# Performance work log

Hardware: AMD Instinct MI355X
Metric: run time of the kernel (lower is better)

## Reference

```python
import jax, jax.numpy as jnp
import numpy as np

B, N_TOK, N_ATOM = 1, 1024, 4096
C_S, C_Z, C_ATOM, C_PAIR = 384, 128, 128, 16
N_QUERY, N_KEY = 32, 128
N_BLOCKS = N_ATOM // N_QUERY
EPS = 1e-5


def layer_norm_scale(x, w):
    # LayerNorm with create_offset=False (scale only)
    mu = jnp.mean(x, axis=-1, keepdims=True)
    var = jnp.mean(jnp.square(x - mu), axis=-1, keepdims=True)
    return (x - mu) * jax.lax.rsqrt(var + EPS) * w


def atom_to_token_idx(num_atoms):
    # num_atoms: [N_tok] int -> token index for each atom [N_ATOM]
    ends = jnp.cumsum(num_atoms)
    return jnp.searchsorted(ends, jnp.arange(N_ATOM), side='right')


def setup_inputs() -> dict:
    key = jax.random.key(0)
    ks = jax.random.split(key, 10)
    return {
        'token_mask': jnp.ones((B, N_TOK), jnp.float32),
        'num_atoms_per_token': jnp.full((B, N_TOK), N_ATOM // N_TOK, jnp.int32),
        'cl': jax.random.normal(ks[0], (B, N_ATOM, C_ATOM), jnp.float32),
        'plm': jax.random.normal(ks[1], (B, N_BLOCKS, N_QUERY, N_KEY, C_PAIR), jnp.float32),
        'si_trunk': jax.random.normal(ks[2], (B, N_TOK, C_S), jnp.float32),
        'zij_trunk': jax.random.normal(ks[3], (B, N_TOK, N_TOK, C_Z), jnp.float32),
        'rl': jax.random.normal(ks[4], (B, N_ATOM, 3), jnp.float32),
        'ln_s_w': jnp.ones((C_S,), jnp.float32),
        'W_s': jax.random.normal(ks[5], (C_S, C_ATOM), jnp.float32) * 0.02,
        'b_s': jnp.zeros((C_ATOM,), jnp.float32),
        'ln_z_w': jnp.ones((C_Z,), jnp.float32),
        'W_z': jax.random.normal(ks[6], (C_Z, C_PAIR), jnp.float32) * 0.02,
        'b_z': jnp.zeros((C_PAIR,), jnp.float32),
        'W_r': jax.random.normal(ks[7], (3, C_ATOM), jnp.float32) * 0.02,
        'b_r': jnp.zeros((C_ATOM,), jnp.float32),
        'n_query': N_QUERY,
        'n_key': N_KEY,
    }


def reference(token_mask, num_atoms_per_token, cl, plm, si_trunk, zij_trunk, rl,
              ln_s_w, W_s, b_s, ln_z_w, W_z, b_z, W_r, b_r, n_query, n_key):
    # --- single rep: LayerNorm + Linear, then token -> atom broadcast ---
    s = jnp.einsum('btc,cd->btd', layer_norm_scale(si_trunk, ln_s_w), W_s) + b_s
    s = s * token_mask[..., None]  # zero padded tokens
    tok = jax.vmap(atom_to_token_idx)(num_atoms_per_token)  # [B, N_ATOM]
    s_atoms = jnp.take_along_axis(s, tok[..., None], axis=1)  # [B, N_ATOM, c_atom]
    cl_out = cl + s_atoms

    # --- pair rep: LayerNorm + Linear, then pair -> local block gather ---
    z = jnp.einsum('bijc,cd->bijd', layer_norm_scale(zij_trunk, ln_z_w), W_z) + b_z
    n_blocks = N_ATOM // n_query
    q_idx = jnp.arange(n_blocks)[:, None] * n_query + jnp.arange(n_query)[None, :]
    k_off = n_query // 2 - n_key // 2  # key window centered on query block
    k_idx = jnp.arange(n_blocks)[:, None] * n_query + k_off + jnp.arange(n_key)[None, :]
    valid = ((k_idx >= 0) & (k_idx < N_ATOM)).astype(z.dtype)  # [L, n_key]
    k_idx_c = jnp.clip(k_idx, 0, N_ATOM - 1)
    tok_q = tok[:, q_idx]    # [B, L, n_query]
    tok_k = tok[:, k_idx_c]  # [B, L, n_key]

    def gather_blocks(zb, tq, tk):
        return zb[tq[:, :, None], tk[:, None, :]]  # [L, nq, nk, C_PAIR]

    z_blk = jax.vmap(gather_blocks)(z, tok_q, tok_k)
    z_blk = z_blk * valid[None, :, None, :, None]
    plm_out = plm + z_blk

    # --- noisy position projection ---
    ql = cl_out + jnp.einsum('bac,cd->bad', rl, W_r) + b_r
    return cl_out, plm_out, ql
```

## Files before the change

kernel.cpp:

```cpp
#include <hip/hip_runtime.h>

#define N_TOKS 1024
#define N_ATOMS 4096
#define CS 384
#define CZ 128
#define CATOM 128
#define CPAIR 16
#define NQ 32
#define NK 128
#define NBLK 128
#define KOFF (-48)
#define KSEG 32
#define NSEG (NK / KSEG)
#define NB_B (NBLK * NSEG)
#define NB_A 256
#define LN_EPS 1e-5f

union alignas(16) SMem {
    struct {
        float ztile[NQ * KSEG * CPAIR];
        int ends[N_TOKS];
        int tokq[NQ]; int tokk[KSEG];
        int qmap[NQ]; int kmap[KSEG];
        int uqtok[NQ]; int uktok[KSEG];
        float kvalid[KSEG];
        int uqk[2];
        int wsum[4];
    } b;
    struct {
        float xh[CS][4];
        float sacc[8][4][CATOM];
        float s_l[4][CATOM];
        int ends[N_TOKS];
        int wsum[4];
    } a;
};

__device__ __forceinline__ void scan_ends(const int* __restrict__ na, int* ends, int* wsum, int t) {
    int4 v = ((const int4*)na)[t];
    int e0 = v.x, e1 = e0 + v.y, e2 = e1 + v.z, e3 = e2 + v.w;
    int s = e3;
    int lane = t & 63, w = t >> 6;
    #pragma unroll
    for (int off = 1; off < 64; off <<= 1) {
        int u = __shfl_up(s, off);
        if (lane >= off) s += u;
    }
    if (lane == 63) wsum[w] = s;
    __syncthreads();
    int wbase = 0;
    #pragma unroll
    for (int i = 0; i < 4; i++) wbase += (i < w) ? wsum[i] : 0;
    int base = wbase + s - e3;
    ends[4 * t + 0] = base + e0;
    ends[4 * t + 1] = base + e1;
    ends[4 * t + 2] = base + e2;
    ends[4 * t + 3] = base + e3;
    __syncthreads();
}

__device__ __forceinline__ int bsearch_tok(const int* ends, int a) {
    int lo = 0, hi = N_TOKS - 1;
    while (lo < hi) { int mid = (lo + hi) >> 1; if (ends[mid] > a) hi = mid; else lo = mid + 1; }
    return lo;
}

__global__ __launch_bounds__(256) void k_all(
        const int* __restrict__ na, const float* __restrict__ si,
        const float* __restrict__ lnw, const float* __restrict__ Ws,
        const float* __restrict__ bs, const float* __restrict__ mask,
        const float* __restrict__ cl, const float* __restrict__ rl,
        const float* __restrict__ Wr, const float* __restrict__ br,
        const float* __restrict__ zij, const float* __restrict__ lnzw,
        const float* __restrict__ Wz, const float* __restrict__ bz,
        const float* __restrict__ plm,
        float* __restrict__ cl_out, float* __restrict__ ql, float* __restrict__ plm_out) {
    __shared__ SMem sm;
    int t = threadIdx.x;
    int x = blockIdx.x;

    if (x >= NB_B) {
        int b = x - NB_B, Tlo = b * 4;
        scan_ends(na, sm.a.ends, sm.a.wsum, t);
        {
            int tl = t >> 6, l = t & 63;
            const float4* row4 = (const float4*)(si + (size_t)(Tlo + tl) * CS);
            float4 v0 = row4[l];
            float4 v1 = make_float4(0.f, 0.f, 0.f, 0.f);
            if (l < 32) v1 = row4[64 + l];
            float sum = v0.x + v0.y + v0.z + v0.w + v1.x + v1.y + v1.z + v1.w;
            float sq = v0.x*v0.x + v0.y*v0.y + v0.z*v0.z + v0.w*v0.w
                     + v1.x*v1.x + v1.y*v1.y + v1.z*v1.z + v1.w*v1.w;
            #pragma unroll
            for (int m = 32; m >= 1; m >>= 1) { sum += __shfl_xor(sum, m); sq += __shfl_xor(sq, m); }
            float mu = sum * (1.f / CS);
            float rstd = rsqrtf(sq * (1.f / CS) - mu * mu + LN_EPS);
            float4 g0 = ((const float4*)lnw)[l];
            sm.a.xh[4*l+0][tl] = (v0.x - mu) * rstd * g0.x;
            sm.a.xh[4*l+1][tl] = (v0.y - mu) * rstd * g0.y;
            sm.a.xh[4*l+2][tl] = (v0.z - mu) * rstd * g0.z;
            sm.a.xh[4*l+3][tl] = (v0.w - mu) * rstd * g0.w;
            if (l < 32) {
                float4 g1 = ((const float4*)lnw)[64 + l];
                sm.a.xh[256+4*l+0][tl] = (v1.x - mu) * rstd * g1.x;
                sm.a.xh[256+4*l+1][tl] = (v1.y - mu) * rstd * g1.y;
                sm.a.xh[256+4*l+2][tl] = (v1.z - mu) * rstd * g1.z;
                sm.a.xh[256+4*l+3][tl] = (v1.w - mu) * rstd * g1.w;
            }
        }
        __syncthreads();
        {
            int d4 = t & 31, cc = t >> 5;
            float4 a0 = make_float4(0,0,0,0), a1 = a0, a2 = a0, a3 = a0;
            const float4* Ws4 = (const float4*)Ws;
            int c0 = 48 * cc;
            #pragma unroll 4
            for (int c = c0; c < c0 + 48; c++) {
                float4 w = Ws4[(size_t)c * 32 + d4];
                float4 xv = *(const float4*)&sm.a.xh[c][0];
                a0.x += xv.x * w.x; a0.y += xv.x * w.y; a0.z += xv.x * w.z; a0.w += xv.x * w.w;
                a1.x += xv.y * w.x; a1.y += xv.y * w.y; a1.z += xv.y * w.z; a1.w += xv.y * w.w;
                a2.x += xv.z * w.x; a2.y += xv.z * w.y; a2.z += xv.z * w.z; a2.w += xv.z * w.w;
                a3.x += xv.w * w.x; a3.y += xv.w * w.y; a3.z += xv.w * w.z; a3.w += xv.w * w.w;
            }
            *(float4*)&sm.a.sacc[cc][0][d4 * 4] = a0;
            *(float4*)&sm.a.sacc[cc][1][d4 * 4] = a1;
            *(float4*)&sm.a.sacc[cc][2][d4 * 4] = a2;
            *(float4*)&sm.a.sacc[cc][3][d4 * 4] = a3;
        }
        __syncthreads();
        if (t < 128) {
            int tk = t >> 5, d = t & 31;
            float4 a = make_float4(0,0,0,0);
            #pragma unroll
            for (int cc = 0; cc < 8; cc++) {
                float4 p = *(const float4*)&sm.a.sacc[cc][tk][d * 4];
                a.x += p.x; a.y += p.y; a.z += p.z; a.w += p.w;
            }
            float4 bb = ((const float4*)bs)[d];
            float m = mask[Tlo + tk];
            a.x = (a.x + bb.x) * m; a.y = (a.y + bb.y) * m;
            a.z = (a.z + bb.z) * m; a.w = (a.w + bb.w) * m;
            *(float4*)&sm.a.s_l[tk][d * 4] = a;
        }
        __syncthreads();
        int elo = (Tlo == 0) ? 0 : sm.a.ends[Tlo - 1];
        int e_0 = sm.a.ends[Tlo], e_1 = sm.a.ends[Tlo + 1], e_2 = sm.a.ends[Tlo + 2];
        int ehi = (b == NB_A - 1) ? N_ATOMS : sm.a.ends[Tlo + 3];
        elo = min(max(elo, 0), N_ATOMS);
        ehi = min(max(ehi, 0), N_ATOMS);
        if (ehi < elo) ehi = elo;
        int items = (ehi - elo) * 32;
        for (int i = t; i < items; i += 256) {
            int a = elo + (i >> 5), d = i & 31;
            int tk = (a >= e_0) + (a >= e_1) + (a >= e_2);
            float4 c4 = ((const float4*)cl)[(size_t)a * 32 + d];
            float4 sv = *(const float4*)&sm.a.s_l[tk][d * 4];
            float4 co;
            co.x = c4.x + sv.x; co.y = c4.y + sv.y; co.z = c4.z + sv.z; co.w = c4.w + sv.w;
            float px = rl[a * 3 + 0], py = rl[a * 3 + 1], pz = rl[a * 3 + 2];
            float4 w0 = ((const float4*)Wr)[d];
            float4 w1 = ((const float4*)Wr)[32 + d];
            float4 w2 = ((const float4*)Wr)[64 + d];
            float4 bb = ((const float4*)br)[d];
            float4 q;
            q.x = co.x + px * w0.x + py * w1.x + pz * w2.x + bb.x;
            q.y = co.y + px * w0.y + py * w1.y + pz * w2.y + bb.y;
            q.z = co.z + px * w0.z + py * w1.z + pz * w2.z + bb.z;
            q.w = co.w + px * w0.w + py * w1.w + pz * w2.w + bb.w;
            ((float4*)cl_out)[(size_t)a * 32 + d] = co;
            ((float4*)ql)[(size_t)a * 32 + d] = q;
        }
        return;
    }

    int blk = x >> 2, kseg = x & 3;
    scan_ends(na, sm.b.ends, sm.b.wsum, t);

    if (t < NQ) {
        sm.b.tokq[t] = bsearch_tok(sm.b.ends, blk * NQ + t);
    } else if (t >= 64 && t < 64 + KSEG) {
        int kk = t - 64;
        int kg = blk * NQ + KOFF + kseg * KSEG + kk;
        sm.b.kvalid[kk] = (kg >= 0 && kg < N_ATOMS) ? 1.0f : 0.0f;
        sm.b.tokk[kk] = bsearch_tok(sm.b.ends, min(max(kg, 0), N_ATOMS - 1));
    }
    __syncthreads();

    if (t < NQ) {
        int tq = sm.b.tokq[t];
        bool head = (t == 0) || (tq != sm.b.tokq[t - 1]);
        unsigned long long m = __ballot(head);
        int rank = (int)__popcll(m & ((2ull << t) - 1)) - 1;
        sm.b.qmap[t] = rank;
        if (head) sm.b.uqtok[rank] = tq;
        if (t == 0) sm.b.uqk[0] = (int)__popcll(m);
    } else if (t >= 64 && t < 64 + KSEG) {
        int lane = t - 64;
        int tk = sm.b.tokk[lane];
        bool head = (lane == 0) || (tk != sm.b.tokk[lane - 1]);
        unsigned long long m = __ballot(head);
        int rank = (int)__popcll(m & ((2ull << lane) - 1)) - 1;
        sm.b.kmap[lane] = rank;
        if (head) sm.b.uktok[rank] = tk;
        if (lane == 0) sm.b.uqk[1] = (int)__popcll(m);
    }
    __syncthreads();
    int uq = sm.b.uqk[0], uk = sm.b.uqk[1];
    int npairs = uq * uk;

    const float4* plm4 = (const float4*)plm;
    float4 pv[16];
    #pragma unroll
    for (int i = 0; i < 16; i++) {
        int f = t + i * 256;
        int d4 = f & 3;
        int kk = (f >> 2) & 31;
        int q  = f >> 7;
        size_t g = ((size_t)(blk * NQ + q) * NK + (size_t)kseg * KSEG + kk) * (CPAIR / 4) + d4;
        pv[i] = plm4[g];
    }

    for (int p = t; p < npairs; p += 256) {
        int qi = p / uk, ki = p - qi * uk;
        int tq = sm.b.uqtok[qi], tk = sm.b.uktok[ki];
        const float* row = zij + ((size_t)tq * N_TOKS + tk) * CZ;
        float sum = 0.f, sq = 0.f;
        for (int c4 = 0; c4 < CZ / 4; c4++) {
            float4 v = *(const float4*)(row + c4 * 4);
            sum += v.x + v.y + v.z + v.w;
            sq  += v.x * v.x + v.y * v.y + v.z * v.z + v.w * v.w;
        }
        float mu = sum * (1.f / CZ);
        float rstd = rsqrtf(sq * (1.f / CZ) - mu * mu + LN_EPS);
        float acc[CPAIR];
        #pragma unroll
        for (int d = 0; d < CPAIR; d++) acc[d] = bz[d];
        for (int c4 = 0; c4 < CZ / 4; c4++) {
            float4 v = *(const float4*)(row + c4 * 4);
            float xs4[4] = {v.x, v.y, v.z, v.w};
            #pragma unroll
            for (int j = 0; j < 4; j++) {
                int c = c4 * 4 + j;
                float xv = (xs4[j] - mu) * rstd * lnzw[c];
                const float* wrow = Wz + c * CPAIR;
                #pragma unroll
                for (int d = 0; d < CPAIR; d++) acc[d] += xv * wrow[d];
            }
        }
        float* zt = &sm.b.ztile[(qi * KSEG + ki) * CPAIR];
        #pragma unroll
        for (int d = 0; d < CPAIR; d++) zt[d] = acc[d];
    }
    __syncthreads();

    float4* out4 = (float4*)plm_out;
    #pragma unroll
    for (int i = 0; i < 16; i++) {
        int f = t + i * 256;
        int d4 = f & 3;
        int kk = (f >> 2) & 31;
        int q  = f >> 7;
        size_t g = ((size_t)(blk * NQ + q) * NK + (size_t)kseg * KSEG + kk) * (CPAIR / 4) + d4;
        float vd = sm.b.kvalid[kk];
        const float4 z = *(const float4*)&sm.b.ztile[(sm.b.qmap[q] * KSEG + sm.b.kmap[kk]) * CPAIR + d4 * 4];
        float4 v = pv[i];
        v.x += vd * z.x; v.y += vd * z.y; v.z += vd * z.z; v.w += vd * z.w;
        out4[g] = v;
    }
}

extern "C" void kernel_launch(void* const* d_in, const int* in_sizes, int n_in,
                              void* d_out, int out_size, void* d_ws, size_t ws_size,
                              hipStream_t stream) {
    (void)in_sizes; (void)n_in; (void)out_size; (void)d_ws; (void)ws_size;
    const float* token_mask = (const float*)d_in[0];
    const int*   num_atoms  = (const int*)d_in[1];
    const float* cl   = (const float*)d_in[2];
    const float* plm  = (const float*)d_in[3];
    const float* si   = (const float*)d_in[4];
    const float* zij  = (const float*)d_in[5];
    const float* rl   = (const float*)d_in[6];
    const float* ln_s_w = (const float*)d_in[7];
    const float* W_s  = (const float*)d_in[8];
    const float* b_s  = (const float*)d_in[9];
    const float* ln_z_w = (const float*)d_in[10];
    const float* W_z  = (const float*)d_in[11];
    const float* b_z  = (const float*)d_in[12];
    const float* W_r  = (const float*)d_in[13];
    const float* b_r  = (const float*)d_in[14];

    float* out_cl  = (float*)d_out;
    float* out_plm = out_cl + (size_t)N_ATOMS * CATOM;
    float* out_ql  = out_plm + (size_t)NBLK * NQ * NK * CPAIR;

    k_all<<<NB_B + NB_A, 256, 0, stream>>>(num_atoms, si, ln_s_w, W_s, b_s, token_mask,
                                           cl, rl, W_r, b_r,
                                           zij, ln_z_w, W_z, b_z, plm,
                                           out_cl, out_ql, out_plm);
}
```

Measured before the change: 40.00 us.

## Split pair LayerNorm-projection across 8 lanes per pair and halve key segments

Each unique token pair's 128-channel LayerNorm and 128x16 projection is now computed by 8 cooperating lanes, each handling 16 channels, with reductions done by cross-lane shuffles. Previously a single thread handled a whole pair. The key segment shrinks from 32 to 16, doubling the number of pair-path blocks, and the plm prefetch is moved ahead of the token scan so it overlaps with it. Pairs are processed in chunks of up to 256 through shared memory, with an extra sync per chunk. This adds shuffle overhead and recomputes some pairs across the finer segments.

```diff
diff --git a/kernel.cpp b/kernel.cpp
--- a/kernel.cpp
+++ b/kernel.cpp
@@ -10,15 +10,16 @@
 #define NK 128
 #define NBLK 128
 #define KOFF (-48)
-#define KSEG 32
+#define KSEG 16
 #define NSEG (NK / KSEG)
 #define NB_B (NBLK * NSEG)
 #define NB_A 256
+#define MAXP 256
 #define LN_EPS 1e-5f
 
 union alignas(16) SMem {
     struct {
-        float ztile[NQ * KSEG * CPAIR];
+        float ztile[MAXP * CPAIR];
         int ends[N_TOKS];
         int tokq[NQ]; int tokk[KSEG];
         int qmap[NQ]; int kmap[KSEG];
@@ -174,7 +175,20 @@
         return;
     }
 
-    int blk = x >> 2, kseg = x & 3;
+    int blk = x >> 3, kseg = x & 7;
+
+    const float4* plm4 = (const float4*)plm;
+    float4 pv[8];
+    #pragma unroll
+    for (int i = 0; i < 8; i++) {
+        int f = t + i * 256;
+        int d4 = f & 3;
+        int kk = (f >> 2) & 15;
+        int q  = f >> 6;
+        size_t g = ((size_t)(blk * NQ + q) * NK + (size_t)kseg * KSEG + kk) * (CPAIR / 4) + d4;
+        pv[i] = plm4[g];
+    }
+
     scan_ends(na, sm.b.ends, sm.b.wsum, t);
 
     if (t < NQ) {
@@ -209,64 +223,89 @@
     int uq = sm.b.uqk[0], uk = sm.b.uqk[1];
     int npairs = uq * uk;
 
-    const float4* plm4 = (const float4*)plm;
-    float4 pv[16];
+    int sl = t & 7;
+    const float4* bz4 = (const float4*)bz;
+    float4 bz0 = bz4[0], bz1 = bz4[1], bz2 = bz4[2], bz3 = bz4[3];
+
+    for (int c0 = 0; c0 < npairs; c0 += MAXP) {
+        int cend = min(npairs, c0 + MAXP);
+        for (int p = c0 + (t >> 3); p < cend; p += 32) {
+            int qi = p / uk, ki = p - qi * uk;
+            const float4* rp = (const float4*)(zij + ((size_t)sm.b.uqtok[qi] * N_TOKS + sm.b.uktok[ki]) * CZ + sl * 16);
+            float4 v0 = rp[0], v1 = rp[1], v2 = rp[2], v3 = rp[3];
+            float sum = v0.x+v0.y+v0.z+v0.w + v1.x+v1.y+v1.z+v1.w
+                      + v2.x+v2.y+v2.z+v2.w + v3.x+v3.y+v3.z+v3.w;
+            float sq = v0.x*v0.x+v0.y*v0.y+v0.z*v0.z+v0.w*v0.w
+                     + v1.x*v1.x+v1.y*v1.y+v1.z*v1.z+v1.w*v1.w
+                     + v2.x*v2.x+v2.y*v2.y+v2.z*v2.z+v2.w*v2.w
+                     + v3.x*v3.x+v3.y*v3.y+v3.z*v3.z+v3.w*v3.w;
+            sum += __shfl_xor(sum, 1); sq += __shfl_xor(sq, 1);
+            sum += __shfl_xor(sum, 2); sq += __shfl_xor(sq, 2);
+            sum += __shfl_xor(sum, 4); sq += __shfl_xor(sq, 4);
+            float mu = sum * (1.f / CZ);
+            float rstd = rsqrtf(sq * (1.f / CZ) - mu * mu + LN_EPS);
+            const float4* l4 = (const float4*)(lnzw + sl * 16);
+            float4 g0 = l4[0], g1 = l4[1], g2 = l4[2], g3 = l4[3];
+            v0.x = (v0.x-mu)*rstd*g0.x; v0.y = (v0.y-mu)*rstd*g0.y; v0.z = (v0.z-mu)*rstd*g0.z; v0.w = (v0.w-mu)*rstd*g0.w;
+            v1.x = (v1.x-mu)*rstd*g1.x; v1.y = (v1.y-mu)*rstd*g1.y; v1.z = (v1.z-mu)*rstd*g1.z; v1.w = (v1.w-mu)*rstd*g1.w;
+            v2.x = (v2.x-mu)*rstd*g2.x; v2.y = (v2.y-mu)*rstd*g2.y; v2.z = (v2.z-mu)*rstd*g2.z; v2.w = (v2.w-mu)*rstd*g2.w;
+            v3.x = (v3.x-mu)*rstd*g3.x; v3.y = (v3.y-mu)*rstd*g3.y; v3.z = (v3.z-mu)*rstd*g3.z; v3.w = (v3.w-mu)*rstd*g3.w;
+            float acc[16];
+            #pragma unroll
+            for (int d = 0; d < 16; d++) acc[d] = 0.f;
+            const float4* Wp = (const float4*)(Wz + sl * 16 * CPAIR);
+            #define CH(J, XV) { \
+                float4 w0 = Wp[(J)*4+0], w1 = Wp[(J)*4+1], w2 = Wp[(J)*4+2], w3 = Wp[(J)*4+3]; \
+                acc[ 0] += (XV)*w0.x; acc[ 1] += (XV)*w0.y; acc[ 2] += (XV)*w0.z; acc[ 3] += (XV)*w0.w; \
+                acc[ 4] += (XV)*w1.x; acc[ 5] += (XV)*w1.y; acc[ 6] += (XV)*w1.z; acc[ 7] += (XV)*w1.w; \
+                acc[ 8] += (XV)*w2.x; acc[ 9] += (XV)*w2.y; acc[10] += (XV)*w2.z; acc[11] += (XV)*w2.w; \
+                acc[12] += (XV)*w3.x; acc[13] += (XV)*w3.y; acc[14] += (XV)*w3.z; acc[15] += (XV)*w3.w; }
+            CH(0, v0.x) CH(1, v0.y) CH(2, v0.z) CH(3, v0.w)
+            CH(4, v1.x) CH(5, v1.y) CH(6, v1.z) CH(7, v1.w)
+            CH(8, v2.x) CH(9, v2.y) CH(10, v2.z) CH(11, v2.w)
+            CH(12, v3.x) CH(13, v3.y) CH(14, v3.z) CH(15, v3.w)
+            #undef CH
+            #pragma unroll
+            for (int d = 0; d < 16; d++) {
+                acc[d] += __shfl_xor(acc[d], 1);
+                acc[d] += __shfl_xor(acc[d], 2);
+                acc[d] += __shfl_xor(acc[d], 4);
+            }
+            if (sl == 0) {
+                float* zt = &sm.b.ztile[(p - c0) * CPAIR];
+                *(float4*)&zt[ 0] = make_float4(acc[ 0]+bz0.x, acc[ 1]+bz0.y, acc[ 2]+bz0.z, acc[ 3]+bz0.w);
+                *(float4*)&zt[ 4] = make_float4(acc[ 4]+bz1.x, acc[ 5]+bz1.y, acc[ 6]+bz1.z, acc[ 7]+bz1.w);
+                *(float4*)&zt[ 8] = make_float4(acc[ 8]+bz2.x, acc[ 9]+bz2.y, acc[10]+bz2.z, acc[11]+bz2.w);
+                *(float4*)&zt[12] = make_float4(acc[12]+bz3.x, acc[13]+bz3.y, acc[14]+bz3.z, acc[15]+bz3.w);
+            }
+        }
+        __syncthreads();
+        #pragma unroll
+        for (int i = 0; i < 8; i++) {
+            int f = t + i * 256;
+            int d4 = f & 3;
+            int kk = (f >> 2) & 15;
+            int q  = f >> 6;
+            int pidx = sm.b.qmap[q] * uk + sm.b.kmap[kk];
+            if (pidx >= c0 && pidx < cend) {
+                float vd = sm.b.kvalid[kk];
+                const float4 z = *(const float4*)&sm.b.ztile[(pidx - c0) * CPAIR + d4 * 4];
+                pv[i].x += vd * z.x; pv[i].y += vd * z.y;
+                pv[i].z += vd * z.z; pv[i].w += vd * z.w;
+            }
+        }
+        __syncthreads();
+    }
+
+    float4* out4 = (float4*)plm_out;
     #pragma unroll
-    for (int i = 0; i < 16; i++) {
+    for (int i = 0; i < 8; i++) {
         int f = t + i * 256;
         int d4 = f & 3;
-        int kk = (f >> 2) & 31;
-        int q  = f >> 7;
+        int kk = (f >> 2) & 15;
+        int q  = f >> 6;
         size_t g = ((size_t)(blk * NQ + q) * NK + (size_t)kseg * KSEG + kk) * (CPAIR / 4) + d4;
-        pv[i] = plm4[g];
-    }
-
-    for (int p = t; p < npairs; p += 256) {
-        int qi = p / uk, ki = p - qi * uk;
-        int tq = sm.b.uqtok[qi], tk = sm.b.uktok[ki];
-        const float* row = zij + ((size_t)tq * N_TOKS + tk) * CZ;
-        float sum = 0.f, sq = 0.f;
-        for (int c4 = 0; c4 < CZ / 4; c4++) {
-            float4 v = *(const float4*)(row + c4 * 4);
-            sum += v.x + v.y + v.z + v.w;
-            sq  += v.x * v.x + v.y * v.y + v.z * v.z + v.w * v.w;
-        }
-        float mu = sum * (1.f / CZ);
-        float rstd = rsqrtf(sq * (1.f / CZ) - mu * mu + LN_EPS);
-        float acc[CPAIR];
-        #pragma unroll
-        for (int d = 0; d < CPAIR; d++) acc[d] = bz[d];
-        for (int c4 = 0; c4 < CZ / 4; c4++) {
-            float4 v = *(const float4*)(row + c4 * 4);
-            float xs4[4] = {v.x, v.y, v.z, v.w};
-            #pragma unroll
-            for (int j = 0; j < 4; j++) {
-                int c = c4 * 4 + j;
-                float xv = (xs4[j] - mu) * rstd * lnzw[c];
-                const float* wrow = Wz + c * CPAIR;
-                #pragma unroll
-                for (int d = 0; d < CPAIR; d++) acc[d] += xv * wrow[d];
-            }
-        }
-        float* zt = &sm.b.ztile[(qi * KSEG + ki) * CPAIR];
-        #pragma unroll
-        for (int d = 0; d < CPAIR; d++) zt[d] = acc[d];
-    }
-    __syncthreads();
-
-    float4* out4 = (float4*)plm_out;
-    #pragma unroll
-    for (int i = 0; i < 16; i++) {
-        int f = t + i * 256;
-        int d4 = f & 3;
-        int kk = (f >> 2) & 31;
-        int q  = f >> 7;
-        size_t g = ((size_t)(blk * NQ + q) * NK + (size_t)kseg * KSEG + kk) * (CPAIR / 4) + d4;
-        float vd = sm.b.kvalid[kk];
-        const float4 z = *(const float4*)&sm.b.ztile[(sm.b.qmap[q] * KSEG + sm.b.kmap[kk]) * CPAIR + d4 * 4];
-        float4 v = pv[i];
-        v.x += vd * z.x; v.y += vd * z.y; v.z += vd * z.z; v.w += vd * z.w;
-        out4[g] = v;
+        out4[g] = pv[i];
     }
 }
 
```

New measurement: 63.26 us. 1.58x slower.

## Split pair path into compute kernel and separate plm streaming kernel via workspace

Applied to the files above, without the earlier changes.

The fused kernel becomes two kernels. The first computes the projected pair tiles and index maps and writes them to a global workspace. The second kernel, with four times as many blocks, streams plm, adds the gathered z values and writes plm_out. This removes the 16 register-held plm loads per thread and the large shared-memory z tile, which should raise occupancy and parallelism in the bandwidth-bound streaming part. The cost is an extra launch, a workspace write and read-back of z, and no overlap between the zij compute and the plm streaming.

```diff
diff --git a/kernel.cpp b/kernel.cpp
--- a/kernel.cpp
+++ b/kernel.cpp
@@ -12,20 +12,21 @@
 #define KOFF (-48)
 #define KSEG 32
 #define NSEG (NK / KSEG)
-#define NB_B (NBLK * NSEG)
+#define NTILE (NBLK * NSEG)
 #define NB_A 256
+#define MAXP 1024
+#define MAPSTRIDE 68
 #define LN_EPS 1e-5f
 
 union alignas(16) SMem {
     struct {
-        float ztile[NQ * KSEG * CPAIR];
         int ends[N_TOKS];
         int tokq[NQ]; int tokk[KSEG];
         int qmap[NQ]; int kmap[KSEG];
         int uqtok[NQ]; int uktok[KSEG];
-        float kvalid[KSEG];
         int uqk[2];
         int wsum[4];
+        int vmask;
     } b;
     struct {
         float xh[CS][4];
@@ -65,7 +66,7 @@
     return lo;
 }
 
-__global__ __launch_bounds__(256) void k_all(
+__global__ __launch_bounds__(256) void k_pre(
         const int* __restrict__ na, const float* __restrict__ si,
         const float* __restrict__ lnw, const float* __restrict__ Ws,
         const float* __restrict__ bs, const float* __restrict__ mask,
@@ -73,14 +74,14 @@
         const float* __restrict__ Wr, const float* __restrict__ br,
         const float* __restrict__ zij, const float* __restrict__ lnzw,
         const float* __restrict__ Wz, const float* __restrict__ bz,
-        const float* __restrict__ plm,
-        float* __restrict__ cl_out, float* __restrict__ ql, float* __restrict__ plm_out) {
+        float* __restrict__ z_ws, int* __restrict__ maps_ws,
+        float* __restrict__ cl_out, float* __restrict__ ql) {
     __shared__ SMem sm;
     int t = threadIdx.x;
     int x = blockIdx.x;
 
-    if (x >= NB_B) {
-        int b = x - NB_B, Tlo = b * 4;
+    if (x >= NTILE) {
+        int b = x - NTILE, Tlo = b * 4;
         scan_ends(na, sm.a.ends, sm.a.wsum, t);
         {
             int tl = t >> 6, l = t & 63;
@@ -182,7 +183,9 @@
     } else if (t >= 64 && t < 64 + KSEG) {
         int kk = t - 64;
         int kg = blk * NQ + KOFF + kseg * KSEG + kk;
-        sm.b.kvalid[kk] = (kg >= 0 && kg < N_ATOMS) ? 1.0f : 0.0f;
+        bool val = (kg >= 0 && kg < N_ATOMS);
+        unsigned long long vm = __ballot(val);
+        if (kk == 0) sm.b.vmask = (int)(vm & 0xffffffffull);
         sm.b.tokk[kk] = bsearch_tok(sm.b.ends, min(max(kg, 0), N_ATOMS - 1));
     }
     __syncthreads();
@@ -209,17 +212,11 @@
     int uq = sm.b.uqk[0], uk = sm.b.uqk[1];
     int npairs = uq * uk;
 
-    const float4* plm4 = (const float4*)plm;
-    float4 pv[16];
-    #pragma unroll
-    for (int i = 0; i < 16; i++) {
-        int f = t + i * 256;
-        int d4 = f & 3;
-        int kk = (f >> 2) & 31;
-        int q  = f >> 7;
-        size_t g = ((size_t)(blk * NQ + q) * NK + (size_t)kseg * KSEG + kk) * (CPAIR / 4) + d4;
-        pv[i] = plm4[g];
-    }
+    int* mp = maps_ws + x * MAPSTRIDE;
+    if (t < NQ) mp[1 + t] = sm.b.qmap[t];
+    else if (t >= 64 && t < 64 + KSEG) mp[33 + (t - 64)] = sm.b.kmap[t - 64];
+    else if (t == 96) mp[0] = uk;
+    else if (t == 97) mp[65] = sm.b.vmask;
 
     for (int p = t; p < npairs; p += 256) {
         int qi = p / uk, ki = p - qi * uk;
@@ -248,23 +245,48 @@
                 for (int d = 0; d < CPAIR; d++) acc[d] += xv * wrow[d];
             }
         }
-        float* zt = &sm.b.ztile[(qi * KSEG + ki) * CPAIR];
-        #pragma unroll
-        for (int d = 0; d < CPAIR; d++) zt[d] = acc[d];
-    }
-    __syncthreads();
-
+        float4* zt = (float4*)(z_ws + ((size_t)x * MAXP + p) * CPAIR);
+        zt[0] = make_float4(acc[0], acc[1], acc[2], acc[3]);
+        zt[1] = make_float4(acc[4], acc[5], acc[6], acc[7]);
+        zt[2] = make_float4(acc[8], acc[9], acc[10], acc[11]);
+        zt[3] = make_float4(acc[12], acc[13], acc[14], acc[15]);
+    }
+}
+
+__global__ __launch_bounds__(256) void k_stream(
+        const float* __restrict__ z_ws, const int* __restrict__ maps_ws,
+        const float* __restrict__ plm, float* __restrict__ plm_out) {
+    __shared__ int qmap_l[8];
+    __shared__ int kmap_l[32];
+    __shared__ int s_uk, s_vm;
+    int t = threadIdx.x;
+    int b = blockIdx.x;
+    int tau = b >> 2, qq = b & 3;
+    int blk = tau >> 2, kseg = tau & 3;
+
+    const int* mp = maps_ws + tau * MAPSTRIDE;
+    if (t < 32) kmap_l[t] = mp[33 + t];
+    else if (t < 40) qmap_l[t - 32] = mp[1 + qq * 8 + (t - 32)];
+    else if (t == 40) s_uk = mp[0];
+    else if (t == 41) s_vm = mp[65];
+    __syncthreads();
+    int uk = s_uk, vm = s_vm;
+
+    const float4* plm4 = (const float4*)plm;
+    const float4* z4 = (const float4*)z_ws;
     float4* out4 = (float4*)plm_out;
     #pragma unroll
-    for (int i = 0; i < 16; i++) {
+    for (int i = 0; i < 4; i++) {
         int f = t + i * 256;
         int d4 = f & 3;
         int kk = (f >> 2) & 31;
         int q  = f >> 7;
-        size_t g = ((size_t)(blk * NQ + q) * NK + (size_t)kseg * KSEG + kk) * (CPAIR / 4) + d4;
-        float vd = sm.b.kvalid[kk];
-        const float4 z = *(const float4*)&sm.b.ztile[(sm.b.qmap[q] * KSEG + sm.b.kmap[kk]) * CPAIR + d4 * 4];
-        float4 v = pv[i];
+        int grow = blk * NQ + qq * 8 + q;
+        size_t g = ((size_t)grow * NK + kseg * KSEG + kk) * 4 + d4;
+        float4 v = plm4[g];
+        int pidx = qmap_l[q] * uk + kmap_l[kk];
+        float4 z = z4[((size_t)tau * MAXP + pidx) * 4 + d4];
+        float vd = ((vm >> kk) & 1) ? 1.0f : 0.0f;
         v.x += vd * z.x; v.y += vd * z.y; v.z += vd * z.z; v.w += vd * z.w;
         out4[g] = v;
     }
@@ -273,7 +295,7 @@
 extern "C" void kernel_launch(void* const* d_in, const int* in_sizes, int n_in,
                               void* d_out, int out_size, void* d_ws, size_t ws_size,
                               hipStream_t stream) {
-    (void)in_sizes; (void)n_in; (void)out_size; (void)d_ws; (void)ws_size;
+    (void)in_sizes; (void)n_in; (void)out_size; (void)ws_size;
     const float* token_mask = (const float*)d_in[0];
     const int*   num_atoms  = (const int*)d_in[1];
     const float* cl   = (const float*)d_in[2];
@@ -294,8 +316,12 @@
     float* out_plm = out_cl + (size_t)N_ATOMS * CATOM;
     float* out_ql  = out_plm + (size_t)NBLK * NQ * NK * CPAIR;
 
-    k_all<<<NB_B + NB_A, 256, 0, stream>>>(num_atoms, si, ln_s_w, W_s, b_s, token_mask,
-                                           cl, rl, W_r, b_r,
-                                           zij, ln_z_w, W_z, b_z, plm,
-                                           out_cl, out_ql, out_plm);
-}
+    float* z_ws    = (float*)d_ws;
+    int*   maps_ws = (int*)((char*)d_ws + (size_t)NTILE * MAXP * CPAIR * 4);
+
+    k_pre<<<NTILE + NB_A, 256, 0, stream>>>(num_atoms, si, ln_s_w, W_s, b_s, token_mask,
+                                            cl, rl, W_r, b_r,
+                                            zij, ln_z_w, W_z, b_z,
+                                            z_ws, maps_ws, out_cl, out_ql);
+    k_stream<<<NTILE * 4, 256, 0, stream>>>(z_ws, maps_ws, plm, out_plm);
+}
```

After: 35.53 us. -11.2%, faster.

## Split pair-block work across 4x more blocks by query subgroups

Applied to the files above, without the earlier changes.

Each block now handles an 8-query by 32-key sub-tile instead of 32 by 32, so the pair phase launches four times as many workgroups. The z tile in shared memory is indexed compactly by unique pair, and the key validity flags become a ballot bitmask. The aim is more parallelism and lower per-block latency. The cost is that every block repeats the token-end scan and binary searches, so setup work is duplicated four times.

```diff
diff --git a/kernel.cpp b/kernel.cpp
--- a/kernel.cpp
+++ b/kernel.cpp
@@ -11,21 +11,22 @@
 #define NBLK 128
 #define KOFF (-48)
 #define KSEG 32
-#define NSEG (NK / KSEG)
-#define NB_B (NBLK * NSEG)
+#define QSUB 8
+#define NB_B (NBLK * 16)
 #define NB_A 256
+#define MAXP 256
 #define LN_EPS 1e-5f
 
 union alignas(16) SMem {
     struct {
-        float ztile[NQ * KSEG * CPAIR];
+        float ztile[MAXP * CPAIR];
         int ends[N_TOKS];
-        int tokq[NQ]; int tokk[KSEG];
-        int qmap[NQ]; int kmap[KSEG];
-        int uqtok[NQ]; int uktok[KSEG];
-        float kvalid[KSEG];
+        int tokq[QSUB]; int tokk[KSEG];
+        int qmap[QSUB]; int kmap[KSEG];
+        int uqtok[QSUB]; int uktok[KSEG];
         int uqk[2];
         int wsum[4];
+        int vmask;
     } b;
     struct {
         float xh[CS][4];
@@ -174,20 +175,21 @@
         return;
     }
 
-    int blk = x >> 2, kseg = x & 3;
+    int blk = x >> 4, kseg = (x >> 2) & 3, qq = x & 3;
     scan_ends(na, sm.b.ends, sm.b.wsum, t);
 
-    if (t < NQ) {
-        sm.b.tokq[t] = bsearch_tok(sm.b.ends, blk * NQ + t);
+    if (t < QSUB) {
+        sm.b.tokq[t] = bsearch_tok(sm.b.ends, blk * NQ + qq * QSUB + t);
     } else if (t >= 64 && t < 64 + KSEG) {
         int kk = t - 64;
         int kg = blk * NQ + KOFF + kseg * KSEG + kk;
-        sm.b.kvalid[kk] = (kg >= 0 && kg < N_ATOMS) ? 1.0f : 0.0f;
+        unsigned long long vm = __ballot(kg >= 0 && kg < N_ATOMS);
+        if (kk == 0) sm.b.vmask = (int)(vm & 0xffffffffull);
         sm.b.tokk[kk] = bsearch_tok(sm.b.ends, min(max(kg, 0), N_ATOMS - 1));
     }
     __syncthreads();
 
-    if (t < NQ) {
+    if (t < QSUB) {
         int tq = sm.b.tokq[t];
         bool head = (t == 0) || (tq != sm.b.tokq[t - 1]);
         unsigned long long m = __ballot(head);
@@ -210,19 +212,19 @@
     int npairs = uq * uk;
 
     const float4* plm4 = (const float4*)plm;
-    float4 pv[16];
+    float4 pv[4];
     #pragma unroll
-    for (int i = 0; i < 16; i++) {
+    for (int i = 0; i < 4; i++) {
         int f = t + i * 256;
         int d4 = f & 3;
         int kk = (f >> 2) & 31;
         int q  = f >> 7;
-        size_t g = ((size_t)(blk * NQ + q) * NK + (size_t)kseg * KSEG + kk) * (CPAIR / 4) + d4;
+        size_t g = ((size_t)(blk * NQ + qq * QSUB + q) * NK + kseg * KSEG + kk) * 4 + d4;
         pv[i] = plm4[g];
     }
 
-    for (int p = t; p < npairs; p += 256) {
-        int qi = p / uk, ki = p - qi * uk;
+    if (t < npairs) {
+        int qi = t / uk, ki = t - qi * uk;
         int tq = sm.b.uqtok[qi], tk = sm.b.uktok[ki];
         const float* row = zij + ((size_t)tq * N_TOKS + tk) * CZ;
         float sum = 0.f, sq = 0.f;
@@ -248,22 +250,24 @@
                 for (int d = 0; d < CPAIR; d++) acc[d] += xv * wrow[d];
             }
         }
-        float* zt = &sm.b.ztile[(qi * KSEG + ki) * CPAIR];
+        float* zt = &sm.b.ztile[t * CPAIR];
         #pragma unroll
         for (int d = 0; d < CPAIR; d++) zt[d] = acc[d];
     }
     __syncthreads();
 
+    int vm = sm.b.vmask;
     float4* out4 = (float4*)plm_out;
     #pragma unroll
-    for (int i = 0; i < 16; i++) {
+    for (int i = 0; i < 4; i++) {
         int f = t + i * 256;
         int d4 = f & 3;
         int kk = (f >> 2) & 31;
         int q  = f >> 7;
-        size_t g = ((size_t)(blk * NQ + q) * NK + (size_t)kseg * KSEG + kk) * (CPAIR / 4) + d4;
-        float vd = sm.b.kvalid[kk];
-        const float4 z = *(const float4*)&sm.b.ztile[(sm.b.qmap[q] * KSEG + sm.b.kmap[kk]) * CPAIR + d4 * 4];
+        size_t g = ((size_t)(blk * NQ + qq * QSUB + q) * NK + kseg * KSEG + kk) * 4 + d4;
+        int pidx = sm.b.qmap[q] * uk + sm.b.kmap[kk];
+        const float4 z = *(const float4*)&sm.b.ztile[pidx * CPAIR + d4 * 4];
+        float vd = ((vm >> kk) & 1) ? 1.0f : 0.0f;
         float4 v = pv[i];
         v.x += vd * z.x; v.y += vd * z.y; v.z += vd * z.z; v.w += vd * z.w;
         out4[g] = v;
```

New measurement: 48.42 us. 1.21x slower.
